# Kernel optimization log

Measured on AMD Instinct MI355X. Metric: run time of the kernel, lower is better.

The kernel has to match this reference:

```python
import jax, jax.numpy as jnp
import numpy as np

B, C, T = 16, 512, 1024      # batch, in_shape (channels), seq_len
H, D = 8, 64                 # num_heads, head_dim; embed = H*D == C
E = H * D
EPS = 1e-6


def setup_inputs() -> dict:
    key = jax.random.key(0)
    ks = jax.random.split(key, 10)
    s_in = 1.0 / np.sqrt(C)
    s_e = 1.0 / np.sqrt(E)
    return {
        "X": jax.random.normal(ks[0], (B, C, T), jnp.float32),
        "ln_g": jnp.ones((C,), jnp.float32),
        "ln_b": jnp.zeros((C,), jnp.float32),
        "Wq": jax.random.normal(ks[1], (C, E), jnp.float32) * s_in,
        "bq": jnp.zeros((E,), jnp.float32),
        "Wk": jax.random.normal(ks[2], (C, E), jnp.float32) * s_in,
        "bk": jnp.zeros((E,), jnp.float32),
        "Wv": jax.random.normal(ks[3], (C, E), jnp.float32) * s_in,
        "bv": jnp.zeros((E,), jnp.float32),
        "Wo": jax.random.normal(ks[4], (E, C), jnp.float32) * s_e,
        "bo": jnp.zeros((C,), jnp.float32),
    }


def reference(X, ln_g, ln_b, Wq, bq, Wk, bk, Wv, bv, Wo, bo):
    # dimshuffle: (B, C, T) -> (B, T, C)
    x = jnp.transpose(X, (0, 2, 1))
    # pre-norm LayerNorm over last dim, eps=1e-6
    mu = jnp.mean(x, axis=-1, keepdims=True)
    var = jnp.mean(jnp.square(x - mu), axis=-1, keepdims=True)
    xn = (x - mu) * jax.lax.rsqrt(var + EPS) * ln_g + ln_b
    # QKV projections, split into heads: (B, T, H, D)
    q = (xn @ Wq + bq).reshape(B, T, H, D)
    k = (xn @ Wk + bk).reshape(B, T, H, D)
    v = (xn @ Wv + bv).reshape(B, T, H, D)
    # attention: scores (B, H, T, T)
    scores = jnp.einsum("bqhd,bkhd->bhqk", q, k) / np.sqrt(D)
    w = jax.nn.softmax(scores, axis=-1)
    h = jnp.einsum("bhqk,bkhd->bqhd", w, v).reshape(B, T, E)
    out = h @ Wo + bo            # output projection (dropout=0 in eval)
    out = x + out                # residual
    return jnp.transpose(out, (0, 2, 1))  # back to (B, C, T)
```

## Files before the change

### kernel.cpp

```cpp
#include <hip/hip_runtime.h>
#include <hip/hip_bf16.h>
#include <cstdint>
#include <cstddef>

typedef __attribute__((ext_vector_type(8))) __bf16 bf16x8;
typedef __attribute__((ext_vector_type(4))) float f32x4;
typedef __attribute__((ext_vector_type(16))) float f32x16;
typedef __attribute__((ext_vector_type(4))) unsigned short u16x4;
typedef __attribute__((ext_vector_type(4))) unsigned int u32x4;
typedef unsigned int u32;

#define NB 16
#define NC 512
#define NT 1024
#define NH 8
#define ND 64
#define NE 512

__device__ __forceinline__ void gld16(void* lds, const void* g) {
  __builtin_amdgcn_global_load_lds(
      (const __attribute__((address_space(1))) u32*)g,
      (__attribute__((address_space(3))) u32*)lds, 16, 0, 0);
}

__device__ __forceinline__ unsigned short f2bf(float f) {
  __bf16 h = (__bf16)f;
  return __builtin_bit_cast(unsigned short, h);
}

__device__ __forceinline__ float ex2(float x) {
  float r; asm("v_exp_f32 %0, %1" : "=v"(r) : "v"(x)); return r;
}

__device__ __forceinline__ void pl32swap(u32& a, u32& b) {
  asm("v_permlane32_swap_b32 %0, %1" : "+v"(a), "+v"(b));
}

__global__ __launch_bounds__(256) void wt_convert4(
    const float* __restrict__ Wq, const float* __restrict__ Wk,
    const float* __restrict__ Wv, const float* __restrict__ Wo,
    __bf16* __restrict__ Wtq, __bf16* __restrict__ Wtk,
    __bf16* __restrict__ Wtv, __bf16* __restrict__ Wto)
{
  __shared__ float tile[32][33];
  const int w = blockIdx.y;
  const float* W = (w == 0) ? Wq : (w == 1) ? Wk : (w == 2) ? Wv : Wo;
  __bf16*     Wt = (w == 0) ? Wtq : (w == 1) ? Wtk : (w == 2) ? Wtv : Wto;
  const int bx = blockIdx.x & 15, by = blockIdx.x >> 4;
  const int r0 = by * 32, c0 = bx * 32;
  const int tx = threadIdx.x & 31, ty = threadIdx.x >> 5;
#pragma unroll
  for (int i = 0; i < 4; i++)
    tile[ty + i * 8][tx] = W[(size_t)(r0 + ty + i * 8) * 512 + c0 + tx];
  __syncthreads();
#pragma unroll
  for (int i = 0; i < 4; i++) {
    const int cc = ty + i * 8;
    Wt[(size_t)(c0 + cc) * 512 + r0 + tx] = (__bf16)tile[tx][cc];
  }
}

__global__ __launch_bounds__(256) void ln_kernel(
    const float* __restrict__ X, const float* __restrict__ gam,
    const float* __restrict__ bet, __bf16* __restrict__ xn)
{
  __shared__ float tile[16][513];
  __shared__ float mu_s[16], rs_s[16];
  const int b  = blockIdx.x >> 6;
  const int t0 = (blockIdx.x & 63) << 4;
  const int tid = threadIdx.x;
  const int tl = tid & 15, c0 = tid >> 4;
  const float* Xb = X + (size_t)b * NC * NT + t0;
  for (int c = c0; c < NC; c += 16)
    tile[tl][c] = Xb[(size_t)c * NT + tl];
  __syncthreads();
  const int row = tid >> 4, sub = tid & 15;
  float s = 0.f, s2 = 0.f;
  for (int c = sub; c < NC; c += 16) { const float v = tile[row][c]; s += v; s2 += v * v; }
  s += __shfl_xor(s, 1);  s2 += __shfl_xor(s2, 1);
  s += __shfl_xor(s, 2);  s2 += __shfl_xor(s2, 2);
  s += __shfl_xor(s, 4);  s2 += __shfl_xor(s2, 4);
  s += __shfl_xor(s, 8);  s2 += __shfl_xor(s2, 8);
  const float mu   = s * (1.f / NC);
  const float var  = s2 * (1.f / NC) - mu * mu;
  const float rstd = rsqrtf(var + 1e-6f);
  if (sub == 0) { mu_s[row] = mu; rs_s[row] = rstd; }
  __syncthreads();
  __bf16* xo = xn + ((size_t)b * NT + t0) * NC;
  for (int i = tid; i < 16 * NC; i += 256) {
    const int r = i >> 9, c = i & (NC - 1);
    xo[(size_t)r * NC + c] = (__bf16)((tile[r][c] - mu_s[r]) * rs_s[r] * gam[c] + bet[c]);
  }
}

__global__ __launch_bounds__(256) void gemm_qkv(
    const __bf16* __restrict__ A, const __bf16* __restrict__ Wt,
    const float* __restrict__ bq, const float* __restrict__ bk, const float* __restrict__ bv,
    __bf16* __restrict__ qb, __bf16* __restrict__ kb, __bf16* __restrict__ vtb)
{
  __shared__ __align__(16) __bf16 lA[128 * 32];
  __shared__ __align__(16) __bf16 lB[128 * 32];
  __shared__ float tb[4][16][17];
  const int tid = threadIdx.x;
  const int wv = tid >> 6, lane = tid & 63;
  const int bid = blockIdx.x;
  const int mchunk = bid / 192, rem = bid % 192;
  const int xcd = rem & 7, loc = rem >> 3;
  const int mt = mchunk * 16 + xcd * 2 + (loc / 12);
  const int nt = loc % 12;
  const int m0 = mt << 7, n0 = nt << 7;
  const int fr = lane & 15, kq = lane >> 4;
  const int wr = wv >> 1, wc = wv & 1;

  const __bf16* Ag0 = A + (size_t)(m0 + (tid >> 2)) * NC + (tid & 3) * 8;
  const __bf16* Ag1 = Ag0 + (size_t)64 * NC;
  const __bf16* Bg0 = Wt + (size_t)(n0 + (tid >> 2)) * NC + (tid & 3) * 8;
  const __bf16* Bg1 = Bg0 + (size_t)64 * NC;
  __bf16* lA0 = lA + wv * 512; __bf16* lA1 = lA + 2048 + wv * 512;
  __bf16* lB0 = lB + wv * 512; __bf16* lB1 = lB + 2048 + wv * 512;

  f32x4 acc[4][4] = {};
  for (int k0 = 0; k0 < NC; k0 += 32) {
    gld16(lA0, Ag0 + k0); gld16(lA1, Ag1 + k0);
    gld16(lB0, Bg0 + k0); gld16(lB1, Bg1 + k0);
    __syncthreads();
    bf16x8 af[4], bfr[4];
#pragma unroll
    for (int i = 0; i < 4; i++) {
      af[i]  = *(const bf16x8*)&lA[(wr * 64 + i * 16 + fr) * 32 + kq * 8];
      bfr[i] = *(const bf16x8*)&lB[(wc * 64 + i * 16 + fr) * 32 + kq * 8];
    }
#pragma unroll
    for (int i = 0; i < 4; i++)
#pragma unroll
      for (int j = 0; j < 4; j++)
        acc[i][j] = __builtin_amdgcn_mfma_f32_16x16x32_bf16(af[i], bfr[j], acc[i][j], 0, 0, 0);
    __syncthreads();
  }

  const int wsel = n0 >> 9;
  const float* bias = (wsel == 0) ? bq : (wsel == 1) ? bk : bv;
  const float qsc = (wsel == 0) ? 0.18033688011112042f : 1.0f;
  if (wsel < 2) {
#pragma unroll
    for (int i = 0; i < 4; i++) {
#pragma unroll
      for (int j = 0; j < 4; j++) {
        const int ng = (n0 & 511) + wc * 64 + j * 16 + fr;
        const int hh = ng >> 6, dd = ng & 63;
        const float bb = bias[ng];
#pragma unroll
        for (int r = 0; r < 4; r++) {
          const int mg = m0 + wr * 64 + i * 16 + kq * 4 + r;
          const int b = mg >> 10, t = mg & 1023;
          const __bf16 h16 = (__bf16)((acc[i][j][r] + bb) * qsc);
          if (wsel == 0) qb[(((size_t)b * NH + hh) * NT + t) * ND + dd] = h16;
          else           kb[(((size_t)b * NH + hh) * NT + t) * ND + dd] = h16;
        }
      }
    }
  } else {
#pragma unroll
    for (int i = 0; i < 4; i++) {
#pragma unroll
      for (int j = 0; j < 4; j++) {
#pragma unroll
        for (int r = 0; r < 4; r++) tb[wv][kq * 4 + r][fr] = acc[i][j][r];
#pragma unroll
        for (int rr = 0; rr < 4; rr++) {
          const int cloc = kq * 4 + rr;
          const int ng = (n0 & 511) + wc * 64 + j * 16 + cloc;
          const int hh = ng >> 6, dd = ng & 63;
          const int mg = m0 + wr * 64 + i * 16 + fr;
          const int b = mg >> 10, t = mg & 1023;
          vtb[(((size_t)b * NH + hh) * ND + dd) * NT + t] =
              (__bf16)(tb[wv][fr][cloc] + bias[ng]);
        }
      }
    }
  }
}

__global__ __launch_bounds__(128, 2) void attn_kernel(
    const __bf16* __restrict__ qb, const __bf16* __restrict__ kb,
    const __bf16* __restrict__ vtb, __bf16* __restrict__ hb)
{
  __shared__ __align__(16) __bf16 lK[2][4096];
  __shared__ __align__(16) __bf16 lV[2][4096];
  const int tid = threadIdx.x, wv = tid >> 6, lane = tid & 63;
  const int l31 = lane & 31, hi = lane >> 5;
  const int swz = (l31 & 7) << 4;
  const int bid = blockIdx.x;
  const int xcd = bid & 7, idx = bid >> 3;
  const int hbp = xcd * 16 + (idx >> 3);
  const int chunk = idx & 7;
  const int b = hbp >> 3, hh = hbp & 7;
  const int q0 = chunk * 128 + wv * 64;

  const __bf16* Q = qb + ((size_t)b * NH + hh) * NT * ND;
  const char* Kc = (const char*)(kb  + ((size_t)b * NH + hh) * NT * ND);
  const char* Vc = (const char*)(vtb + ((size_t)b * NH + hh) * ND * NT);

  bf16x8 qf[2][4];
#pragma unroll
  for (int qs = 0; qs < 2; qs++)
#pragma unroll
    for (int ds = 0; ds < 4; ds++)
      qf[qs][ds] = *(const bf16x8*)&Q[(size_t)(q0 + qs * 32 + l31) * ND + ds * 16 + hi * 8];

  float l_run[2] = {0.f, 0.f};
  f32x16 O[2][2] = {};
  const f32x16 zz = {};

  auto stage = [&](int nb, int kt64) {
#pragma unroll
    for (int is = 0; is < 4; is++) {
      const int o  = is * 2048 + wv * 1024 + lane * 16;
      const int rr = o >> 7;
      const int cb = (o & 127) ^ ((rr & 7) << 4);
      gld16((char*)&lK[nb][0] + is * 2048 + wv * 1024,
            Kc + (size_t)(kt64 + rr) * 128 + cb);
      gld16((char*)&lV[nb][0] + is * 2048 + wv * 1024,
            Vc + (size_t)rr * 2048 + (size_t)kt64 * 2 + cb);
    }
  };

  stage(0, 0);
  stage(1, 64);

#pragma unroll 1
  for (int ti = 0; ti < 16; ti++) {
    const int cur = ti & 1;
    if (ti < 15) asm volatile("s_waitcnt vmcnt(8)" ::: "memory");
    else         asm volatile("s_waitcnt vmcnt(0)" ::: "memory");
    __builtin_amdgcn_s_barrier();
    __builtin_amdgcn_sched_barrier(0);
    const char* Kb = (const char*)&lK[cur][0];
    const char* Vb = (const char*)&lV[cur][0];

    f32x16 st[2][2];
    __builtin_amdgcn_s_setprio(1);
#pragma unroll
    for (int ks = 0; ks < 2; ks++) {
#pragma unroll
      for (int ds = 0; ds < 4; ds++) {
        const int row = ks * 32 + l31;
        const bf16x8 ka = *(const bf16x8*)
            (Kb + row * 128 + ((ds * 32 + hi * 16) ^ swz));
        if (ds == 0) {
          st[0][ks] = __builtin_amdgcn_mfma_f32_32x32x16_bf16(ka, qf[0][0], zz, 0, 0, 0);
          st[1][ks] = __builtin_amdgcn_mfma_f32_32x32x16_bf16(ka, qf[1][0], zz, 0, 0, 0);
        } else {
          st[0][ks] = __builtin_amdgcn_mfma_f32_32x32x16_bf16(ka, qf[0][ds], st[0][ks], 0, 0, 0);
          st[1][ks] = __builtin_amdgcn_mfma_f32_32x32x16_bf16(ka, qf[1][ds], st[1][ks], 0, 0, 0);
        }
      }
    }
    __builtin_amdgcn_s_setprio(0);

#pragma unroll
    for (int qs = 0; qs < 2; qs++) {
      float rs = 0.f;
      u32 pk[2][4][2];
#pragma unroll
      for (int ks = 0; ks < 2; ks++)
#pragma unroll
        for (int g = 0; g < 4; g++) {
          const float p0 = ex2(st[qs][ks][4 * g + 0]);
          const float p1 = ex2(st[qs][ks][4 * g + 1]);
          const float p2 = ex2(st[qs][ks][4 * g + 2]);
          const float p3 = ex2(st[qs][ks][4 * g + 3]);
          rs += (p0 + p1) + (p2 + p3);
          asm("v_cvt_pk_bf16_f32 %0, %1, %2" : "=v"(pk[ks][g][0]) : "v"(p0), "v"(p1));
          asm("v_cvt_pk_bf16_f32 %0, %1, %2" : "=v"(pk[ks][g][1]) : "v"(p2), "v"(p3));
        }
      rs += __shfl_xor(rs, 32);
      l_run[qs] += rs;

      __builtin_amdgcn_s_setprio(1);
#pragma unroll
      for (int s = 0; s < 4; s++) {
        const int t = s >> 1, m = s & 1;
        u32 a0 = pk[t][2 * m][0], b0 = pk[t][2 * m + 1][0];
        u32 a1 = pk[t][2 * m][1], b1 = pk[t][2 * m + 1][1];
        pl32swap(a0, b0);
        pl32swap(a1, b1);
        u32x4 w;
        w[0] = a0; w[1] = a1; w[2] = b0; w[3] = b1;
        const bf16x8 pfrag = __builtin_bit_cast(bf16x8, w);
#pragma unroll
        for (int dsub = 0; dsub < 2; dsub++) {
          const int row = dsub * 32 + l31;
          const bf16x8 vf = *(const bf16x8*)
              (Vb + row * 128 + ((s * 32 + hi * 16) ^ swz));
          O[qs][dsub] = __builtin_amdgcn_mfma_f32_32x32x16_bf16(vf, pfrag, O[qs][dsub], 0, 0, 0);
        }
      }
      __builtin_amdgcn_s_setprio(0);
    }

    __builtin_amdgcn_s_barrier();
    __builtin_amdgcn_sched_barrier(0);
    if (ti + 2 < 16) stage(cur, (ti + 2) * 64);
  }

#pragma unroll
  for (int qs = 0; qs < 2; qs++) {
    const float linv = 1.f / l_run[qs];
    const int t = q0 + qs * 32 + l31;
    __bf16* hrow = hb + ((size_t)b * NT + t) * NE + hh * ND;
#pragma unroll
    for (int dsub = 0; dsub < 2; dsub++)
#pragma unroll
      for (int g = 0; g < 4; g++) {
        u16x4 ov;
#pragma unroll
        for (int rr = 0; rr < 4; rr++) ov[rr] = f2bf(O[qs][dsub][4 * g + rr] * linv);
        *(u16x4*)&hrow[dsub * 32 + g * 8 + hi * 4] = ov;
      }
  }
}

__global__ __launch_bounds__(256) void gemm_out(
    const __bf16* __restrict__ A, const __bf16* __restrict__ Wt,
    const float* __restrict__ bo, const float* __restrict__ X,
    float* __restrict__ out)
{
  __shared__ __align__(16) __bf16 lA[128 * 32];
  __shared__ __align__(16) __bf16 lB[128 * 32];
  __shared__ float tb[4][16][17];
  const int tid = threadIdx.x, wv = tid >> 6, lane = tid & 63;
  const int bid = blockIdx.x;
  const int mt = ((bid >> 5) << 3) + (bid & 7);
  const int nt = (bid & 31) >> 3;
  const int m0 = mt << 7, n0 = nt << 7;
  const int fr = lane & 15, kq = lane >> 4;
  const int wr = wv >> 1, wc = wv & 1;

  const __bf16* Ag0 = A + (size_t)(m0 + (tid >> 2)) * NE + (tid & 3) * 8;
  const __bf16* Ag1 = Ag0 + (size_t)64 * NE;
  const __bf16* Bg0 = Wt + (size_t)(n0 + (tid >> 2)) * NE + (tid & 3) * 8;
  const __bf16* Bg1 = Bg0 + (size_t)64 * NE;
  __bf16* lA0 = lA + wv * 512; __bf16* lA1 = lA + 2048 + wv * 512;
  __bf16* lB0 = lB + wv * 512; __bf16* lB1 = lB + 2048 + wv * 512;

  f32x4 acc[4][4] = {};
  for (int k0 = 0; k0 < NE; k0 += 32) {
    gld16(lA0, Ag0 + k0); gld16(lA1, Ag1 + k0);
    gld16(lB0, Bg0 + k0); gld16(lB1, Bg1 + k0);
    __syncthreads();
    bf16x8 af[4], bfr[4];
#pragma unroll
    for (int i = 0; i < 4; i++) {
      af[i]  = *(const bf16x8*)&lA[(wr * 64 + i * 16 + fr) * 32 + kq * 8];
      bfr[i] = *(const bf16x8*)&lB[(wc * 64 + i * 16 + fr) * 32 + kq * 8];
    }
#pragma unroll
    for (int i = 0; i < 4; i++)
#pragma unroll
      for (int j = 0; j < 4; j++)
        acc[i][j] = __builtin_amdgcn_mfma_f32_16x16x32_bf16(af[i], bfr[j], acc[i][j], 0, 0, 0);
    __syncthreads();
  }

#pragma unroll
  for (int i = 0; i < 4; i++) {
#pragma unroll
    for (int j = 0; j < 4; j++) {
#pragma unroll
      for (int r = 0; r < 4; r++) tb[wv][kq * 4 + r][fr] = acc[i][j][r];
#pragma unroll
      for (int rr = 0; rr < 4; rr++) {
        const int cloc = kq * 4 + rr;
        const int mg = m0 + wr * 64 + i * 16 + fr;
        const int b = mg >> 10, t = mg & 1023;
        const int c = n0 + wc * 64 + j * 16 + cloc;
        out[((size_t)b * NC + c) * NT + t] =
            tb[wv][fr][cloc] + bo[c] + X[((size_t)b * NC + c) * NT + t];
      }
    }
  }
}

extern "C" void kernel_launch(void* const* d_in, const int* in_sizes, int n_in,
                              void* d_out, int out_size, void* d_ws, size_t ws_size,
                              hipStream_t stream) {
  const float* X   = (const float*)d_in[0];
  const float* lng = (const float*)d_in[1];
  const float* lnb = (const float*)d_in[2];
  const float* Wq  = (const float*)d_in[3];
  const float* bq  = (const float*)d_in[4];
  const float* Wk  = (const float*)d_in[5];
  const float* bk  = (const float*)d_in[6];
  const float* Wv  = (const float*)d_in[7];
  const float* bv  = (const float*)d_in[8];
  const float* Wo  = (const float*)d_in[9];
  const float* bo  = (const float*)d_in[10];
  float* out = (float*)d_out;

  __bf16* wsb   = (__bf16*)d_ws;
  __bf16* Wtqkv = wsb;
  __bf16* Wot   = wsb + 786432;
  __bf16* xn    = wsb + 1048576;
  __bf16* qbuf  = wsb + 9437184;
  __bf16* kbuf  = wsb + 17825792;
  __bf16* vtbuf = wsb + 26214400;
  __bf16* hbuf  = wsb + 34603008;

  wt_convert4<<<dim3(256, 4), 256, 0, stream>>>(
      Wq, Wk, Wv, Wo, Wtqkv, Wtqkv + 262144, Wtqkv + 524288, Wot);
  ln_kernel<<<NB * (NT / 16), 256, 0, stream>>>(X, lng, lnb, xn);
  gemm_qkv<<<128 * 12, 256, 0, stream>>>(xn, Wtqkv, bq, bk, bv, qbuf, kbuf, vtbuf);
  attn_kernel<<<1024, 128, 0, stream>>>(qbuf, kbuf, vtbuf, hbuf);
  gemm_out<<<128 * 4, 256, 0, stream>>>(hbuf, Wot, bo, X, out);
}
```

Baseline: 142.8 us.

## Use single-wave attention blocks with 32-key tiles and no barriers

The attention kernel moves from 128-thread blocks (two waves sharing K/V tiles) to 64-thread single-wave blocks with twice as many blocks. The K/V tile per stage drops from 64 to 32 keys, with a new LDS swizzle for the narrower V tile. The per-iteration workgroup barriers are removed because each wave now stages its own data. In exchange, each block loads its own K/V, so there is no sharing between waves and global/L2 traffic doubles, and the shorter tiles mean more loop iterations.

```diff
diff --git a/kernel.cpp b/kernel.cpp
--- a/kernel.cpp
+++ b/kernel.cpp
@@ -181,21 +181,22 @@
   }
 }
 
-__global__ __launch_bounds__(128, 2) void attn_kernel(
+__global__ __launch_bounds__(64) void attn_kernel(
     const __bf16* __restrict__ qb, const __bf16* __restrict__ kb,
     const __bf16* __restrict__ vtb, __bf16* __restrict__ hb)
 {
-  __shared__ __align__(16) __bf16 lK[2][4096];
-  __shared__ __align__(16) __bf16 lV[2][4096];
-  const int tid = threadIdx.x, wv = tid >> 6, lane = tid & 63;
+  __shared__ __align__(16) __bf16 lK[2][2048];
+  __shared__ __align__(16) __bf16 lV[2][2048];
+  const int lane = threadIdx.x;
   const int l31 = lane & 31, hi = lane >> 5;
-  const int swz = (l31 & 7) << 4;
+  const int swzK = (l31 & 7) << 4;
+  const int swzV = (l31 & 3) << 4;
   const int bid = blockIdx.x;
   const int xcd = bid & 7, idx = bid >> 3;
-  const int hbp = xcd * 16 + (idx >> 3);
-  const int chunk = idx & 7;
+  const int hbp = xcd * 16 + (idx >> 4);
+  const int chunk = idx & 15;
   const int b = hbp >> 3, hh = hbp & 7;
-  const int q0 = chunk * 128 + wv * 64;
+  const int q0 = chunk * 64;
 
   const __bf16* Q = qb + ((size_t)b * NH + hh) * NT * ND;
   const char* Kc = (const char*)(kb  + ((size_t)b * NH + hh) * NT * ND);
@@ -212,48 +213,50 @@
   f32x16 O[2][2] = {};
   const f32x16 zz = {};
 
-  auto stage = [&](int nb, int kt64) {
+  auto stage = [&](int nb, int kt32) {
 #pragma unroll
     for (int is = 0; is < 4; is++) {
-      const int o  = is * 2048 + wv * 1024 + lane * 16;
-      const int rr = o >> 7;
-      const int cb = (o & 127) ^ ((rr & 7) << 4);
-      gld16((char*)&lK[nb][0] + is * 2048 + wv * 1024,
-            Kc + (size_t)(kt64 + rr) * 128 + cb);
-      gld16((char*)&lV[nb][0] + is * 2048 + wv * 1024,
-            Vc + (size_t)rr * 2048 + (size_t)kt64 * 2 + cb);
+      {
+        const int o  = is * 1024 + lane * 16;
+        const int rr = o >> 7;
+        const int cb = (o & 127) ^ ((rr & 7) << 4);
+        gld16((char*)&lK[nb][0] + is * 1024,
+              Kc + (size_t)(kt32 + rr) * 128 + cb);
+      }
+      {
+        const int o  = is * 1024 + lane * 16;
+        const int rr = o >> 6;
+        const int cb = (o & 63) ^ ((rr & 3) << 4);
+        gld16((char*)&lV[nb][0] + is * 1024,
+              Vc + (size_t)rr * 2048 + (size_t)kt32 * 2 + cb);
+      }
     }
   };
 
   stage(0, 0);
-  stage(1, 64);
+  stage(1, 32);
 
 #pragma unroll 1
-  for (int ti = 0; ti < 16; ti++) {
+  for (int ti = 0; ti < 32; ti++) {
     const int cur = ti & 1;
-    if (ti < 15) asm volatile("s_waitcnt vmcnt(8)" ::: "memory");
+    if (ti < 31) asm volatile("s_waitcnt vmcnt(8)" ::: "memory");
     else         asm volatile("s_waitcnt vmcnt(0)" ::: "memory");
-    __builtin_amdgcn_s_barrier();
     __builtin_amdgcn_sched_barrier(0);
     const char* Kb = (const char*)&lK[cur][0];
     const char* Vb = (const char*)&lV[cur][0];
 
-    f32x16 st[2][2];
+    f32x16 st[2];
     __builtin_amdgcn_s_setprio(1);
 #pragma unroll
-    for (int ks = 0; ks < 2; ks++) {
-#pragma unroll
-      for (int ds = 0; ds < 4; ds++) {
-        const int row = ks * 32 + l31;
-        const bf16x8 ka = *(const bf16x8*)
-            (Kb + row * 128 + ((ds * 32 + hi * 16) ^ swz));
-        if (ds == 0) {
-          st[0][ks] = __builtin_amdgcn_mfma_f32_32x32x16_bf16(ka, qf[0][0], zz, 0, 0, 0);
-          st[1][ks] = __builtin_amdgcn_mfma_f32_32x32x16_bf16(ka, qf[1][0], zz, 0, 0, 0);
-        } else {
-          st[0][ks] = __builtin_amdgcn_mfma_f32_32x32x16_bf16(ka, qf[0][ds], st[0][ks], 0, 0, 0);
-          st[1][ks] = __builtin_amdgcn_mfma_f32_32x32x16_bf16(ka, qf[1][ds], st[1][ks], 0, 0, 0);
-        }
+    for (int ds = 0; ds < 4; ds++) {
+      const bf16x8 ka = *(const bf16x8*)
+          (Kb + l31 * 128 + ((ds * 32 + hi * 16) ^ swzK));
+      if (ds == 0) {
+        st[0] = __builtin_amdgcn_mfma_f32_32x32x16_bf16(ka, qf[0][0], zz, 0, 0, 0);
+        st[1] = __builtin_amdgcn_mfma_f32_32x32x16_bf16(ka, qf[1][0], zz, 0, 0, 0);
+      } else {
+        st[0] = __builtin_amdgcn_mfma_f32_32x32x16_bf16(ka, qf[0][ds], st[0], 0, 0, 0);
+        st[1] = __builtin_amdgcn_mfma_f32_32x32x16_bf16(ka, qf[1][ds], st[1], 0, 0, 0);
       }
     }
     __builtin_amdgcn_s_setprio(0);
@@ -261,28 +264,25 @@
 #pragma unroll
     for (int qs = 0; qs < 2; qs++) {
       float rs = 0.f;
-      u32 pk[2][4][2];
-#pragma unroll
-      for (int ks = 0; ks < 2; ks++)
-#pragma unroll
-        for (int g = 0; g < 4; g++) {
-          const float p0 = ex2(st[qs][ks][4 * g + 0]);
-          const float p1 = ex2(st[qs][ks][4 * g + 1]);
-          const float p2 = ex2(st[qs][ks][4 * g + 2]);
-          const float p3 = ex2(st[qs][ks][4 * g + 3]);
-          rs += (p0 + p1) + (p2 + p3);
-          asm("v_cvt_pk_bf16_f32 %0, %1, %2" : "=v"(pk[ks][g][0]) : "v"(p0), "v"(p1));
-          asm("v_cvt_pk_bf16_f32 %0, %1, %2" : "=v"(pk[ks][g][1]) : "v"(p2), "v"(p3));
-        }
+      u32 pk[4][2];
+#pragma unroll
+      for (int g = 0; g < 4; g++) {
+        const float p0 = ex2(st[qs][4 * g + 0]);
+        const float p1 = ex2(st[qs][4 * g + 1]);
+        const float p2 = ex2(st[qs][4 * g + 2]);
+        const float p3 = ex2(st[qs][4 * g + 3]);
+        rs += (p0 + p1) + (p2 + p3);
+        asm("v_cvt_pk_bf16_f32 %0, %1, %2" : "=v"(pk[g][0]) : "v"(p0), "v"(p1));
+        asm("v_cvt_pk_bf16_f32 %0, %1, %2" : "=v"(pk[g][1]) : "v"(p2), "v"(p3));
+      }
       rs += __shfl_xor(rs, 32);
       l_run[qs] += rs;
 
       __builtin_amdgcn_s_setprio(1);
 #pragma unroll
-      for (int s = 0; s < 4; s++) {
-        const int t = s >> 1, m = s & 1;
-        u32 a0 = pk[t][2 * m][0], b0 = pk[t][2 * m + 1][0];
-        u32 a1 = pk[t][2 * m][1], b1 = pk[t][2 * m + 1][1];
+      for (int s = 0; s < 2; s++) {
+        u32 a0 = pk[2 * s][0], b0 = pk[2 * s + 1][0];
+        u32 a1 = pk[2 * s][1], b1 = pk[2 * s + 1][1];
         pl32swap(a0, b0);
         pl32swap(a1, b1);
         u32x4 w;
@@ -292,16 +292,14 @@
         for (int dsub = 0; dsub < 2; dsub++) {
           const int row = dsub * 32 + l31;
           const bf16x8 vf = *(const bf16x8*)
-              (Vb + row * 128 + ((s * 32 + hi * 16) ^ swz));
+              (Vb + row * 64 + ((s * 32 + hi * 16) ^ swzV));
           O[qs][dsub] = __builtin_amdgcn_mfma_f32_32x32x16_bf16(vf, pfrag, O[qs][dsub], 0, 0, 0);
         }
       }
       __builtin_amdgcn_s_setprio(0);
     }
 
-    __builtin_amdgcn_s_barrier();
-    __builtin_amdgcn_sched_barrier(0);
-    if (ti + 2 < 16) stage(cur, (ti + 2) * 64);
+    if (ti + 2 < 32) stage(cur, (ti + 2) * 32);
   }
 
 #pragma unroll
@@ -411,6 +409,6 @@
       Wq, Wk, Wv, Wo, Wtqkv, Wtqkv + 262144, Wtqkv + 524288, Wot);
   ln_kernel<<<NB * (NT / 16), 256, 0, stream>>>(X, lng, lnb, xn);
   gemm_qkv<<<128 * 12, 256, 0, stream>>>(xn, Wtqkv, bq, bk, bv, qbuf, kbuf, vtbuf);
-  attn_kernel<<<1024, 128, 0, stream>>>(qbuf, kbuf, vtbuf, hbuf);
+  attn_kernel<<<2048, 64, 0, stream>>>(qbuf, kbuf, vtbuf, hbuf);
   gemm_out<<<128 * 4, 256, 0, stream>>>(hbuf, Wot, bo, X, out);
 }
```

Measured after the change: 153.1 us. 1.07x slower.
